# Kernel tuning notes

Hardware: AMD Instinct MI355X
Metric: run time of the kernel (lower is better)

Reference implementation:

```python
import jax, jax.numpy as jnp
import numpy as np

B, DIM, EMBDIM = 32, 512, 512
MEMSIZE, MEMSEQ = 32, 64
VOCAB = 50257


def setup_inputs() -> dict:
    key = jax.random.key(0)
    ks = jax.random.split(key, 10)
    inp = {
        'enc': jax.random.normal(ks[0], (B, DIM), jnp.float32),
        'encsumm': jax.random.normal(ks[1], (B, DIM), jnp.float32),
        'embsumm': jax.random.normal(ks[2], (B, EMBDIM), jnp.float32),
        'memencs': jax.random.normal(ks[3], (B, MEMSIZE, MEMSEQ, DIM), jnp.float32),
        'memencsumm': jax.random.normal(ks[4], (B, MEMSIZE, MEMSEQ, DIM), jnp.float32),
        'memembsumm': jax.random.normal(ks[5], (B, MEMSIZE, MEMSEQ, EMBDIM), jnp.float32),
        'memmask': jnp.ones((B, MEMSIZE, MEMSEQ), jnp.float32),
        'memids': jax.random.randint(ks[6], (B, MEMSIZE, MEMSEQ), 0, VOCAB, jnp.int64 if jax.config.jax_enable_x64 else jnp.int32),
        'W_out': jax.random.normal(ks[7], (VOCAB, 2 * DIM), jnp.float32) * 0.02,
        'b_out': jnp.zeros((VOCAB,), jnp.float32),
        'W_mix': jax.random.normal(ks[8], (2, 2 * DIM), jnp.float32) * 0.02,
        'b_mix': jnp.zeros((2,), jnp.float32),
        'unktok_mask': jnp.ones((VOCAB,), jnp.float32),  # no unktoks
    }
    return inp


def reference(enc, encsumm, embsumm, memencs, memencsumm, memembsumm, memmask,
              memids, W_out, b_out, W_mix, b_mix, unktok_mask):
    # copy branch: attention over flattened memory, scatter-add into vocab
    query = jnp.concatenate([embsumm, jnp.zeros_like(encsumm), enc], axis=-1)        # (B, 2*dim+embdim)
    keys = jnp.concatenate([memembsumm, jnp.zeros_like(memencsumm), memencs], axis=-1)  # (B, M, Z, 2*dim+embdim)
    w = jnp.einsum('bd,bmzd->bmz', query, keys) + jnp.log(memmask)
    b = w.shape[0]
    w = w.reshape(b, -1)                                    # (B, M*Z)
    alphas = jax.nn.softmax(w, axis=-1)
    mem_flat = memencs.reshape(b, -1, memencs.shape[-1])    # (B, M*Z, dim)
    mem_enc_summ = jnp.einsum('bm,bmd->bd', alphas, mem_flat)
    toks = memids.reshape(b, -1)                            # (B, M*Z)
    rows = jnp.arange(b)[:, None]
    vocsize = W_out.shape[0]
    probs_mem = jnp.zeros((b, vocsize), alphas.dtype).at[rows, toks].add(alphas)
    # generation branch
    h = jnp.concatenate([encsumm, enc], axis=-1)            # (B, 2*dim)
    logits_gen = h @ W_out.T + b_out + jnp.log(unktok_mask)[None, :]
    probs_gen = jax.nn.softmax(logits_gen, axis=-1)
    # mixer combine
    mix = jax.nn.softmax(h @ W_mix.T + b_mix, axis=-1)      # (B, 2)
    probs = mix[:, 0:1] * probs_gen + mix[:, 1:2] * probs_mem
    # original stack/gather trick: selects probs where nonzero, zeros where zero -> identity
    probs = jnp.where(probs != 0, probs, jnp.zeros_like(probs))
    return probs, mem_enc_summ
```

## Files before the change

kernel.cpp:

```cpp
#include <hip/hip_runtime.h>
#include <hip/hip_bf16.h>

#define NB   32
#define DIMK 512
#define MM   32
#define ZZ   64
#define MZV  2048
#define VOC  50257

typedef __attribute__((ext_vector_type(8))) short  short8;
typedef __attribute__((ext_vector_type(4))) float  f32x4;
typedef __attribute__((ext_vector_type(8))) unsigned short ushort8;

#define WS_W      0
#define WS_PVEC   (WS_W + NB*MZV)
#define WS_LSTAT  (WS_PVEC + NB*MM*DIMK)
#define WS_GSTATW (WS_LSTAT + NB*MM*2)
#define WS_MIX    (WS_GSTATW + NB*2)
#define WS_GPART  (WS_MIX + NB*2)
#define WS_H      (WS_GPART + NB*32*2)

__device__ __forceinline__ ushort8 cvt8(float4 a, float4 b) {
    union { ushort8 u; __hip_bfloat162 h[4]; } r;
    r.h[0] = __float22bfloat162_rn(make_float2(a.x, a.y));
    r.h[1] = __float22bfloat162_rn(make_float2(a.z, a.w));
    r.h[2] = __float22bfloat162_rn(make_float2(b.x, b.y));
    r.h[3] = __float22bfloat162_rn(make_float2(b.z, b.w));
    return r.u;
}

__global__ void k0_stageh(const float* __restrict__ encsumm, const float* __restrict__ enc,
                          float* __restrict__ ws)
{
    int b = blockIdx.x;
    int c = threadIdx.x * 4;
    const float* src = (c < DIMK) ? (encsumm + b*DIMK + c) : (enc + b*DIMK + (c - DIMK));
    float4 v = *(const float4*)src;
    union { ushort4 u; __hip_bfloat162 h[2]; } o;
    o.h[0] = __float22bfloat162_rn(make_float2(v.x, v.y));
    o.h[1] = __float22bfloat162_rn(make_float2(v.z, v.w));
    *(ushort4*)((unsigned short*)(ws + WS_H) + b*1024 + c) = o.u;
}

__global__ __launch_bounds__(256) void k1_mem(
    const float* __restrict__ enc, const float* __restrict__ embsumm,
    const float* __restrict__ memencs, const float* __restrict__ memembsumm,
    const float* __restrict__ memmask, float* __restrict__ ws)
{
    int blk = blockIdx.x;
    int b = blk >> 5, m = blk & 31;
    int tid = threadIdx.x, wid = tid >> 6, lane = tid & 63;
    int c0 = lane * 4, c1 = c0 + 256;
    const float* encb = enc + b * DIMK;
    const float* embb = embsumm + b * DIMK;
    float4 qe0 = *(const float4*)(encb + c0);
    float4 qe1 = *(const float4*)(encb + c1);
    float4 qm0 = *(const float4*)(embb + c0);
    float4 qm1 = *(const float4*)(embb + c1);
    const float* meb = memencs    + (long)(b*MM + m) * ZZ * DIMK;
    const float* mmb = memembsumm + (long)(b*MM + m) * ZZ * DIMK;
    const float* mkb = memmask    + (long)(b*MM + m) * ZZ;
    float* w_ws = ws + WS_W + b*MZV + m*ZZ;

    float lmax = -3.0e38f, lsum = 0.f;
    float4 a0 = make_float4(0.f,0.f,0.f,0.f), a1 = make_float4(0.f,0.f,0.f,0.f);

    for (int z = wid; z < ZZ; z += 4) {
        const float* mer = meb + z*DIMK;
        const float* mmr = mmb + z*DIMK;
        float4 e0 = *(const float4*)(mer + c0);
        float4 e1 = *(const float4*)(mer + c1);
        float4 s0 = *(const float4*)(mmr + c0);
        float4 s1 = *(const float4*)(mmr + c1);
        float d = e0.x*qe0.x + e0.y*qe0.y + e0.z*qe0.z + e0.w*qe0.w
                + e1.x*qe1.x + e1.y*qe1.y + e1.z*qe1.z + e1.w*qe1.w
                + s0.x*qm0.x + s0.y*qm0.y + s0.z*qm0.z + s0.w*qm0.w
                + s1.x*qm1.x + s1.y*qm1.y + s1.z*qm1.z + s1.w*qm1.w;
        #pragma unroll
        for (int off = 32; off; off >>= 1) d += __shfl_xor(d, off);
        d += logf(mkb[z]);
        if (lane == 0) w_ws[z] = d;
        float nm = fmaxf(lmax, d);
        float sc = __expf(lmax - nm);
        float e  = __expf(d - nm);
        lsum = lsum * sc + e;
        a0.x = a0.x*sc + e*e0.x; a0.y = a0.y*sc + e*e0.y;
        a0.z = a0.z*sc + e*e0.z; a0.w = a0.w*sc + e*e0.w;
        a1.x = a1.x*sc + e*e1.x; a1.y = a1.y*sc + e*e1.y;
        a1.z = a1.z*sc + e*e1.z; a1.w = a1.w*sc + e*e1.w;
        lmax = nm;
    }

    __shared__ float sacc[4][DIMK];
    __shared__ float sst[4][2];
    *(float4*)&sacc[wid][c0] = a0;
    *(float4*)&sacc[wid][c1] = a1;
    if (lane == 0) { sst[wid][0] = lmax; sst[wid][1] = lsum; }
    __syncthreads();
    float bm = fmaxf(fmaxf(sst[0][0], sst[1][0]), fmaxf(sst[2][0], sst[3][0]));
    float sc0 = __expf(sst[0][0]-bm), sc1 = __expf(sst[1][0]-bm);
    float sc2 = __expf(sst[2][0]-bm), sc3 = __expf(sst[3][0]-bm);
    float bs = sst[0][1]*sc0 + sst[1][1]*sc1 + sst[2][1]*sc2 + sst[3][1]*sc3;
    int d0 = tid * 2;
    float2 v0 = *(float2*)&sacc[0][d0];
    float2 v1 = *(float2*)&sacc[1][d0];
    float2 v2 = *(float2*)&sacc[2][d0];
    float2 v3 = *(float2*)&sacc[3][d0];
    float p0 = v0.x*sc0 + v1.x*sc1 + v2.x*sc2 + v3.x*sc3;
    float p1 = v0.y*sc0 + v1.y*sc1 + v2.y*sc2 + v3.y*sc3;
    float* pv = ws + WS_PVEC + (long)(b*MM+m)*DIMK + d0;
    pv[0] = p0; pv[1] = p1;
    if (tid == 0) { float* ls = ws + WS_LSTAT + (b*MM+m)*2; ls[0] = bm; ls[1] = bs; }
}

__global__ __launch_bounds__(256) void k2_comb(
    const float* __restrict__ encsumm, const float* __restrict__ enc,
    const float* __restrict__ W_mix, const float* __restrict__ b_mix,
    float* __restrict__ out, float* __restrict__ ws)
{
    int b = blockIdx.x, tid = threadIdx.x;
    const float* ls = ws + WS_LSTAT + b*MM*2;
    float gm = -3.0e38f;
    #pragma unroll
    for (int m = 0; m < MM; m++) gm = fmaxf(gm, ls[m*2]);
    float gs = 0.f;
    #pragma unroll
    for (int m = 0; m < MM; m++) gs += ls[m*2+1] * __expf(ls[m*2] - gm);
    if (tid == 0) { ws[WS_GSTATW + b*2] = gm; ws[WS_GSTATW + b*2 + 1] = gs; }
    float inv = 1.0f / gs;
    int d0 = tid * 2;
    float p0 = 0.f, p1 = 0.f;
    for (int m = 0; m < MM; m++) {
        float sc = __expf(ls[m*2] - gm);
        const float* pv = ws + WS_PVEC + (long)(b*MM+m)*DIMK + d0;
        p0 += pv[0]*sc; p1 += pv[1]*sc;
    }
    out[(long)NB*VOC + b*DIMK + d0]     = p0 * inv;
    out[(long)NB*VOC + b*DIMK + d0 + 1] = p1 * inv;

    if (tid < 64) {
        int l = tid;
        float m0 = 0.f, m1 = 0.f;
        #pragma unroll
        for (int p = 0; p < 4; p++) {
            int cc = l*4 + p*256;
            float4 h4 = (cc < 512) ? *(const float4*)(encsumm + b*DIMK + cc)
                                   : *(const float4*)(enc + b*DIMK + cc - 512);
            float4 w0 = *(const float4*)(W_mix + cc);
            float4 w1 = *(const float4*)(W_mix + 1024 + cc);
            m0 += h4.x*w0.x + h4.y*w0.y + h4.z*w0.z + h4.w*w0.w;
            m1 += h4.x*w1.x + h4.y*w1.y + h4.z*w1.z + h4.w*w1.w;
        }
        #pragma unroll
        for (int off = 32; off; off >>= 1) { m0 += __shfl_xor(m0, off); m1 += __shfl_xor(m1, off); }
        if (l == 0) {
            m0 += b_mix[0]; m1 += b_mix[1];
            float mx = fmaxf(m0, m1);
            float e0 = __expf(m0-mx), e1 = __expf(m1-mx);
            float s = e0 + e1;
            ws[WS_MIX + b*2] = e0/s; ws[WS_MIX + b*2 + 1] = e1/s;
        }
    }
}

__global__ __launch_bounds__(256, 6) void k4_gemm(
    const unsigned short* __restrict__ hbf,
    const float* __restrict__ W_out, const float* __restrict__ b_out,
    const float* __restrict__ unk, float* __restrict__ logits)
{
    __shared__ __align__(16) unsigned short b_lds[2][8*32*8];
    __shared__ __align__(16) unsigned short a_lds[2][8*32*8];
    int tid = threadIdx.x, wid = tid >> 6, lane = tid & 63;
    int wv = wid >> 1, wb = wid & 1;
    int vt = blockIdx.x * 32;

    int r = tid >> 3, gq = tid & 7;
    long grow = min(vt + r, VOC - 1);
    const float* wbase = W_out + grow * 1024 + gq * 8;
    const unsigned short* abase = hbf + r * 1024 + gq * 8;

    int lg = lane >> 4, ln = lane & 15;

    f32x4 acc = {0.f,0.f,0.f,0.f};
    float4 f0, f1; ushort8 av;

    int bw = (gq*32 + (r ^ ((gq & 3) << 2))) * 8;
    int aw = (gq*32 + (r ^ gq)) * 8;

#define LOADC(c) do { const float* wp = wbase + (c)*64;            \
        f0 = *(const float4*)(wp); f1 = *(const float4*)(wp+4);    \
        av = *(const ushort8*)(abase + (c)*64); } while (0)
#define WRITEC(buf) do {                            \
        *(ushort8*)&b_lds[buf][bw] = cvt8(f0, f1);  \
        *(ushort8*)&a_lds[buf][aw] = av; } while (0)

    LOADC(0); WRITEC(0);
    LOADC(1);
    __syncthreads();

    for (int c = 0; c < 16; ++c) {
        int buf = c & 1;
        #pragma unroll
        for (int s = 0; s < 2; ++s) {
            int g = s*4 + lg;
            short8 bfrag = *(const short8*)&b_lds[buf][(g*32 + ((wv*16 + ln) ^ ((g & 3) << 2)))*8];
            short8 afrag = *(const short8*)&a_lds[buf][(g*32 + ((wb*16 + ln) ^ g))*8];
            acc = __builtin_amdgcn_mfma_f32_16x16x32_bf16(afrag, bfrag, acc, 0, 0, 0);
        }
        if (c < 15) {
            WRITEC(buf ^ 1);
            if (c < 14) LOADC(c + 2);
        }
        __syncthreads();
    }
#undef LOADC
#undef WRITEC

    int v = vt + wv*16 + ln;
    if (v < VOC) {
        float bias = b_out[v] + logf(unk[v]);
        #pragma unroll
        for (int rr = 0; rr < 4; ++rr) {
            int m = wb*16 + lg*4 + rr;
            logits[(long)m*VOC + v] = acc[rr] + bias;
        }
    }
}

__global__ __launch_bounds__(256) void k5_gstat(const float* __restrict__ logits, float* __restrict__ ws)
{
    int chunk = blockIdx.x, b = blockIdx.y, tid = threadIdx.x;
    const int CH = (VOC + 31) / 32;
    int v0 = chunk * CH;
    int v1 = min(VOC, v0 + CH);
    float m = -3.0e38f, s = 0.f;
    for (int v = v0 + tid; v < v1; v += 256) {
        float x = logits[(long)b*VOC + v];
        float nm = fmaxf(m, x);
        s = s*__expf(m - nm) + __expf(x - nm);
        m = nm;
    }
    #pragma unroll
    for (int off = 32; off; off >>= 1) {
        float om = __shfl_xor(m, off), os = __shfl_xor(s, off);
        float nm = fmaxf(m, om);
        s = s*__expf(m - nm) + os*__expf(om - nm);
        m = nm;
    }
    __shared__ float sm[4], ssum[4];
    int wid = tid >> 6, lane = tid & 63;
    if (lane == 0) { sm[wid] = m; ssum[wid] = s; }
    __syncthreads();
    if (tid == 0) {
        float gm = fmaxf(fmaxf(sm[0], sm[1]), fmaxf(sm[2], sm[3]));
        float gs = ssum[0]*__expf(sm[0]-gm) + ssum[1]*__expf(sm[1]-gm)
                 + ssum[2]*__expf(sm[2]-gm) + ssum[3]*__expf(sm[3]-gm);
        ws[WS_GPART + (b*32 + chunk)*2]     = gm;
        ws[WS_GPART + (b*32 + chunk)*2 + 1] = gs;
    }
}

__global__ __launch_bounds__(256) void k6_final(float* __restrict__ probs, const float* __restrict__ ws)
{
    int v = blockIdx.x*256 + threadIdx.x;
    int b = blockIdx.y;
    float gm = -3.0e38f;
    #pragma unroll
    for (int i = 0; i < 32; ++i) gm = fmaxf(gm, ws[WS_GPART + (b*32+i)*2]);
    float gs = 0.f;
    #pragma unroll
    for (int i = 0; i < 32; ++i)
        gs += ws[WS_GPART + (b*32+i)*2 + 1] * __expf(ws[WS_GPART + (b*32+i)*2] - gm);
    if (v >= VOC) return;
    float mix0 = ws[WS_MIX + b*2];
    long idx = (long)b*VOC + v;
    probs[idx] = mix0 * __expf(probs[idx] - gm) / gs;
}

__global__ __launch_bounds__(256) void k7_scatter(const int* __restrict__ memids,
                                                  const float* __restrict__ ws,
                                                  float* __restrict__ probs)
{
    int idx = blockIdx.x*256 + threadIdx.x;
    int b = idx >> 11, mz = idx & 2047;
    float gm = ws[WS_GSTATW + b*2], gs = ws[WS_GSTATW + b*2 + 1];
    float mix1 = ws[WS_MIX + b*2 + 1];
    float alpha = __expf(ws[WS_W + b*MZV + mz] - gm) / gs;
    int tok = memids[b*MZV + mz];
    atomicAdd(&probs[(long)b*VOC + tok], mix1 * alpha);
}

extern "C" void kernel_launch(void* const* d_in, const int* in_sizes, int n_in,
                              void* d_out, int out_size, void* d_ws, size_t ws_size,
                              hipStream_t stream)
{
    const float* enc        = (const float*)d_in[0];
    const float* encsumm    = (const float*)d_in[1];
    const float* embsumm    = (const float*)d_in[2];
    const float* memencs    = (const float*)d_in[3];
    const float* memembsumm = (const float*)d_in[5];
    const float* memmask    = (const float*)d_in[6];
    const int*   memids     = (const int*)d_in[7];
    const float* W_out      = (const float*)d_in[8];
    const float* b_out      = (const float*)d_in[9];
    const float* W_mix      = (const float*)d_in[10];
    const float* b_mix      = (const float*)d_in[11];
    const float* unk        = (const float*)d_in[12];
    float* out = (float*)d_out;
    float* ws  = (float*)d_ws;

    hipLaunchKernelGGL(k0_stageh, dim3(NB), dim3(256), 0, stream, encsumm, enc, ws);
    hipLaunchKernelGGL(k1_mem, dim3(NB*MM), dim3(256), 0, stream,
                       enc, embsumm, memencs, memembsumm, memmask, ws);
    hipLaunchKernelGGL(k2_comb, dim3(NB), dim3(256), 0, stream,
                       encsumm, enc, W_mix, b_mix, out, ws);
    hipLaunchKernelGGL(k4_gemm, dim3((VOC + 31)/32), dim3(256), 0, stream,
                       (const unsigned short*)(ws + WS_H), W_out, b_out, unk, out);
    hipLaunchKernelGGL(k5_gstat, dim3(32, NB), dim3(256), 0, stream, out, ws);
    hipLaunchKernelGGL(k6_final, dim3((VOC + 255)/256, NB), dim3(256), 0, stream, out, ws);
    hipLaunchKernelGGL(k7_scatter, dim3(NB*MZV/256), dim3(256), 0, stream, memids, ws, out);
}
```

Measured before the change: 140.6 us.

## Stream W_out tiles into LDS with async global_load_lds in logits GEMM

The vocab GEMM now copies fp32 W_out and bf16 h tiles straight into LDS with 16-byte global_load_lds instructions instead of loading them into registers and writing them back. A two-stage buffer is refilled right after each barrier. Conversion of W to bf16 moves to fragment-read time, using an XOR-swizzled fp32 LDS layout. This is meant to cut register staging and VALU work on the bandwidth-bound W_out stream and to keep more loads in flight, at the cost of twice the LDS footprint for W. Correctness depends on the barrier also waiting for the outstanding LDS-DMA loads.

```diff
diff --git a/kernel.cpp b/kernel.cpp
--- a/kernel.cpp
+++ b/kernel.cpp
@@ -27,6 +27,12 @@
     r.h[2] = __float22bfloat162_rn(make_float2(b.x, b.y));
     r.h[3] = __float22bfloat162_rn(make_float2(b.z, b.w));
     return r.u;
+}
+
+typedef const __attribute__((address_space(1))) void* gas_t;
+typedef __attribute__((address_space(3))) void*       las_t;
+__device__ __forceinline__ void gload16(const void* g, void* l) {
+    __builtin_amdgcn_global_load_lds((gas_t)g, (las_t)l, 16, 0, 0);
 }
 
 __global__ void k0_stageh(const float* __restrict__ encsumm, const float* __restrict__ enc,
@@ -168,55 +174,55 @@
     const float* __restrict__ W_out, const float* __restrict__ b_out,
     const float* __restrict__ unk, float* __restrict__ logits)
 {
-    __shared__ __align__(16) unsigned short b_lds[2][8*32*8];
-    __shared__ __align__(16) unsigned short a_lds[2][8*32*8];
+    __shared__ __align__(16) float          w_lds[2][32*64];
+    __shared__ __align__(16) unsigned short a_lds[2][32*64];
     int tid = threadIdx.x, wid = tid >> 6, lane = tid & 63;
     int wv = wid >> 1, wb = wid & 1;
     int vt = blockIdx.x * 32;
 
-    int r = tid >> 3, gq = tid & 7;
-    long grow = min(vt + r, VOC - 1);
-    const float* wbase = W_out + grow * 1024 + gq * 8;
-    const unsigned short* abase = hbf + r * 1024 + gq * 8;
+    int idx0 = (wid*2 + 0)*64 + lane;
+    int idx1 = (wid*2 + 1)*64 + lane;
+    int wr0 = idx0 >> 4, wq0 = idx0 & 15;
+    int wr1 = idx1 >> 4, wq1 = idx1 & 15;
+    const float* wsrc0 = W_out + (long)min(vt + wr0, VOC-1)*1024 + ((wq0 ^ (wr0 & 7))*4);
+    const float* wsrc1 = W_out + (long)min(vt + wr1, VOC-1)*1024 + ((wq1 ^ (wr1 & 7))*4);
+    int aidx = wid*64 + lane;
+    int ar = aidx >> 3, ag = aidx & 7;
+    const unsigned short* asrc = hbf + ar*1024 + ((ag ^ (ar & 7))*8);
+
+#define ISSUE(c, buf) do {                                        \
+        gload16(wsrc0 + (c)*64, &w_lds[buf][idx0*4]);             \
+        gload16(wsrc1 + (c)*64, &w_lds[buf][idx1*4]);             \
+        gload16(asrc  + (c)*64, &a_lds[buf][aidx*8]); } while (0)
 
     int lg = lane >> 4, ln = lane & 15;
-
-    f32x4 acc = {0.f,0.f,0.f,0.f};
-    float4 f0, f1; ushort8 av;
-
-    int bw = (gq*32 + (r ^ ((gq & 3) << 2))) * 8;
-    int aw = (gq*32 + (r ^ gq)) * 8;
-
-#define LOADC(c) do { const float* wp = wbase + (c)*64;            \
-        f0 = *(const float4*)(wp); f1 = *(const float4*)(wp+4);    \
-        av = *(const ushort8*)(abase + (c)*64); } while (0)
-#define WRITEC(buf) do {                            \
-        *(ushort8*)&b_lds[buf][bw] = cvt8(f0, f1);  \
-        *(ushort8*)&a_lds[buf][aw] = av; } while (0)
-
-    LOADC(0); WRITEC(0);
-    LOADC(1);
+    int vrow = wv*16 + ln;
+    int ab   = wb*16 + ln;
+    f32x4 acc = {0.f, 0.f, 0.f, 0.f};
+
+    ISSUE(0, 0);
+    ISSUE(1, 1);
     __syncthreads();
 
     for (int c = 0; c < 16; ++c) {
         int buf = c & 1;
         #pragma unroll
         for (int s = 0; s < 2; ++s) {
+            int q = s*8 + lg*2;
+            float4 b0 = *(const float4*)&w_lds[buf][vrow*64 + ((q    ) ^ (vrow & 7))*4];
+            float4 b1 = *(const float4*)&w_lds[buf][vrow*64 + ((q + 1) ^ (vrow & 7))*4];
             int g = s*4 + lg;
-            short8 bfrag = *(const short8*)&b_lds[buf][(g*32 + ((wv*16 + ln) ^ ((g & 3) << 2)))*8];
-            short8 afrag = *(const short8*)&a_lds[buf][(g*32 + ((wb*16 + ln) ^ g))*8];
+            short8 afrag = *(const short8*)&a_lds[buf][ab*64 + ((g ^ (ab & 7)))*8];
+            ushort8 bu = cvt8(b0, b1);
+            short8 bfrag = *(short8*)&bu;
             acc = __builtin_amdgcn_mfma_f32_16x16x32_bf16(afrag, bfrag, acc, 0, 0, 0);
         }
-        if (c < 15) {
-            WRITEC(buf ^ 1);
-            if (c < 14) LOADC(c + 2);
-        }
         __syncthreads();
-    }
-#undef LOADC
-#undef WRITEC
-
-    int v = vt + wv*16 + ln;
+        if (c + 2 < 16) ISSUE(c + 2, buf);
+    }
+#undef ISSUE
+
+    int v = vt + vrow;
     if (v < VOC) {
         float bias = b_out[v] + logf(unk[v]);
         #pragma unroll
```

New measurement: 141.5 us. Within noise of the previous version (+0.7%).
